# Kernel tuning notes

Measured on AMD Instinct MI355X. Metric: run time of the kernel, lower is better.

Reference implementation:

```python
import jax, jax.numpy as jnp
import numpy as np

N, E, C = 100000, 500000, 128
LN_EPS = 1e-5


def setup_inputs() -> dict:
    key = jax.random.key(0)
    ks = jax.random.split(key, 6)
    x = jax.random.normal(ks[0], (N, C), dtype=jnp.float32)
    edge_index = jax.random.randint(ks[1], (2, E), 0, N, dtype=jnp.int32)
    edge_weight = jax.random.uniform(ks[2], (E,), dtype=jnp.float32)
    scale = 1.0 / np.sqrt(C)
    W1 = jax.random.normal(ks[3], (C, C), dtype=jnp.float32) * scale
    W2 = jax.random.normal(ks[4], (C, C), dtype=jnp.float32) * scale
    b1 = jnp.zeros((C,), jnp.float32)
    b2 = jnp.zeros((C,), jnp.float32)
    g1 = jnp.ones((C,), jnp.float32)
    g2 = jnp.ones((C,), jnp.float32)
    beta1 = jnp.zeros((C,), jnp.float32)
    beta2 = jnp.zeros((C,), jnp.float32)
    return {"x": x, "edge_index": edge_index, "edge_weight": edge_weight,
            "W1": W1, "b1": b1, "g1": g1, "beta1": beta1,
            "W2": W2, "b2": b2, "g2": g2, "beta2": beta2}


def _gcn_norm(edge_index, edge_weight, n):
    # add self loops (weight 1.0), then symmetric deg^{-1/2} normalization;
    # degree() in the source counts edges into col (unweighted), incl. self loops
    src = jnp.concatenate([edge_index[0], jnp.arange(n, dtype=edge_index.dtype)])
    dst = jnp.concatenate([edge_index[1], jnp.arange(n, dtype=edge_index.dtype)])
    ew = jnp.concatenate([edge_weight, jnp.ones((n,), edge_weight.dtype)])
    deg = jax.ops.segment_sum(jnp.ones_like(ew), dst, num_segments=n)
    dis = jnp.where(deg > 0, jax.lax.rsqrt(jnp.maximum(deg, 1.0)) * (deg > 0), 0.0)
    w = dis[src] * ew * dis[dst]
    return src, dst, w


def _layernorm(y, g, b):
    mu = jnp.mean(y, axis=-1, keepdims=True)
    var = jnp.mean(jnp.square(y - mu), axis=-1, keepdims=True)
    return (y - mu) * jax.lax.rsqrt(var + LN_EPS) * g + b


def _gcn_layer(x, W, bias, src, dst, w, n):
    h = x @ W                               # [N,C] linear (no bias)
    msg = w[:, None] * h[src]               # gather + edge scaling [E+N,C]
    out = jax.ops.segment_sum(msg, dst, num_segments=n)  # scatter-add
    return out + bias


def reference(x, edge_index, edge_weight, W1, b1, g1, beta1, W2, b2, g2, beta2):
    n = x.shape[0]
    src, dst, w = _gcn_norm(edge_index, edge_weight, n)
    identity = x
    h = _gcn_layer(x, W1, b1, src, dst, w, n)
    h = jax.nn.gelu(_layernorm(h, g1, beta1), approximate=False)
    h = _gcn_layer(h, W2, b2, src, dst, w, n)
    h = jax.nn.gelu(_layernorm(h, g2, beta2), approximate=False)
    return h + identity
```

## Files before the change

### kernel.cpp

```cpp
#include <hip/hip_runtime.h>
#include <math.h>

#define C 128
#define CAPF 1024
#define CAPA 512

typedef __attribute__((ext_vector_type(8))) short short8;
typedef __attribute__((ext_vector_type(4))) float f32x4;
typedef __attribute__((ext_vector_type(4))) unsigned short ushort4_t;
typedef __attribute__((ext_vector_type(8))) unsigned short ushort8_t;

__device__ inline unsigned short f2b(float f) {
    union { float f; unsigned int u; } v; v.f = f;
    unsigned int u = v.u;
    return (unsigned short)((u + 0x7FFFu + ((u >> 16) & 1u)) >> 16);
}
__device__ inline float bits2f(unsigned int u) {
    union { unsigned int u; float f; } v; v.u = u; return v.f;
}

__device__ inline void acc8(float* a, uint4 u, float s) {
    a[0] += s * bits2f(u.x << 16); a[1] += s * bits2f(u.x & 0xFFFF0000u);
    a[2] += s * bits2f(u.y << 16); a[3] += s * bits2f(u.y & 0xFFFF0000u);
    a[4] += s * bits2f(u.z << 16); a[5] += s * bits2f(u.z & 0xFFFF0000u);
    a[6] += s * bits2f(u.w << 16); a[7] += s * bits2f(u.w & 0xFFFF0000u);
}

__device__ inline void agg_row_lds(
    int row, int c0, int kbeg, int kend, int eb0, int cap,
    const int2* __restrict__ eds, const int2* __restrict__ edata,
    const unsigned short* __restrict__ Hb, const float* __restrict__ dis,
    const float* __restrict__ bias, const float* __restrict__ g,
    const float* __restrict__ beta, float* t) {
    float a[8] = {0.f, 0.f, 0.f, 0.f, 0.f, 0.f, 0.f, 0.f};

    {
        float d = dis[row];
        uint4 hu = *(const uint4*)(Hb + (size_t)row * C + c0);
        acc8(a, hu, d * d);
    }

    const int kc = kend < cap ? kend : cap;
    int k = kbeg;
    for (; k + 3 < kc; k += 4) {
        int2 e0 = eds[k];
        int2 e1 = eds[k + 1];
        int2 e2 = eds[k + 2];
        int2 e3 = eds[k + 3];
        uint4 u0 = *(const uint4*)(Hb + (size_t)e0.x * C + c0);
        uint4 u1 = *(const uint4*)(Hb + (size_t)e1.x * C + c0);
        uint4 u2 = *(const uint4*)(Hb + (size_t)e2.x * C + c0);
        uint4 u3 = *(const uint4*)(Hb + (size_t)e3.x * C + c0);
        acc8(a, u0, bits2f((unsigned int)e0.y));
        acc8(a, u1, bits2f((unsigned int)e1.y));
        acc8(a, u2, bits2f((unsigned int)e2.y));
        acc8(a, u3, bits2f((unsigned int)e3.y));
    }
    for (; k < kc; ++k) {
        int2 e0 = eds[k];
        uint4 u0 = *(const uint4*)(Hb + (size_t)e0.x * C + c0);
        acc8(a, u0, bits2f((unsigned int)e0.y));
    }
    for (; k < kend; ++k) {
        int2 e0 = edata[eb0 + k];
        uint4 u0 = *(const uint4*)(Hb + (size_t)e0.x * C + c0);
        acc8(a, u0, bits2f((unsigned int)e0.y));
    }

    float4 bv0 = *(const float4*)(bias + c0);
    float4 bv1 = *(const float4*)(bias + c0 + 4);
    a[0] += bv0.x; a[1] += bv0.y; a[2] += bv0.z; a[3] += bv0.w;
    a[4] += bv1.x; a[5] += bv1.y; a[6] += bv1.z; a[7] += bv1.w;

    float s = 0.f, sq = 0.f;
    #pragma unroll
    for (int j = 0; j < 8; ++j) { s += a[j]; sq += a[j] * a[j]; }
    #pragma unroll
    for (int off = 8; off >= 1; off >>= 1) {
        s  += __shfl_xor(s, off, 64);
        sq += __shfl_xor(sq, off, 64);
    }
    float mu = s * (1.0f / C);
    float var = sq * (1.0f / C) - mu * mu;
    float rstd = rsqrtf(var + 1e-5f);

    float4 gv0 = *(const float4*)(g + c0);
    float4 gv1 = *(const float4*)(g + c0 + 4);
    float4 be0 = *(const float4*)(beta + c0);
    float4 be1 = *(const float4*)(beta + c0 + 4);
    float gg[8] = {gv0.x, gv0.y, gv0.z, gv0.w, gv1.x, gv1.y, gv1.z, gv1.w};
    float bb[8] = {be0.x, be0.y, be0.z, be0.w, be1.x, be1.y, be1.z, be1.w};

    #pragma unroll
    for (int j = 0; j < 8; ++j) {
        float v = (a[j] - mu) * rstd * gg[j] + bb[j];
        t[j] = 0.5f * v * (1.0f + erff(v * 0.70710678118654752f));
    }
}


__global__ void k_zero(int* __restrict__ cnt, int n) {
    int i = blockIdx.x * blockDim.x + threadIdx.x;
    if (i < n) cnt[i] = 0;
}

__global__ void k_cnt(const int* __restrict__ dst, int* __restrict__ cnt, int e) {
    int i = blockIdx.x * blockDim.x + threadIdx.x;
    if (i < e) atomicAdd(&cnt[dst[i]], 1);
}

__global__ __launch_bounds__(256) void k_scan_a(const int* __restrict__ cnt,
                                                int* __restrict__ rowbeg,
                                                int* __restrict__ blocksum, int n) {
    const int tid = threadIdx.x;
    const int i = blockIdx.x * 256 + tid;
    const int lane = tid & 63, wv = tid >> 6;
    int v = (i < n) ? cnt[i] : 0;
    int x = v;
    #pragma unroll
    for (int off = 1; off < 64; off <<= 1) {
        int y = __shfl_up(x, off, 64);
        if (lane >= off) x += y;
    }
    __shared__ int wsum[4];
    if (lane == 63) wsum[wv] = x;
    __syncthreads();
    int woff = 0;
    #pragma unroll
    for (int k = 0; k < 4; ++k) if (k < wv) woff += wsum[k];
    int incl = x + woff;
    if (i < n) rowbeg[i] = incl - v;
    if (tid == 255) blocksum[blockIdx.x] = incl;
}

__global__ __launch_bounds__(512) void k_scan_b(int* __restrict__ bs, int nb) {
    const int tid = threadIdx.x;
    __shared__ int s[512];
    int v = (tid < nb) ? bs[tid] : 0;
    s[tid] = v;
    __syncthreads();
    for (int off = 1; off < 512; off <<= 1) {
        int t = 0;
        if (tid >= off) t = s[tid - off];
        __syncthreads();
        s[tid] += t;
        __syncthreads();
    }
    if (tid < nb) bs[tid] = s[tid] - v;
}

__global__ void k_scan_c(const int* __restrict__ cnt, const int* __restrict__ bs,
                         int* __restrict__ rowbeg, int* __restrict__ rowcur,
                         float* __restrict__ dis, int n) {
    int i = blockIdx.x * blockDim.x + threadIdx.x;
    if (i >= n) return;
    int rb = rowbeg[i] + bs[i >> 8];
    rowbeg[i] = rb;
    rowcur[i] = rb;
    dis[i] = rsqrtf((float)cnt[i] + 1.0f);
    if (i == n - 1) rowbeg[n] = rb + cnt[i];
}

__global__ void k_place(const int* __restrict__ src, const int* __restrict__ dst,
                        const float* __restrict__ ew, const float* __restrict__ dis,
                        int* __restrict__ rowcur, int2* __restrict__ edata, int e) {
    int i = blockIdx.x * blockDim.x + threadIdx.x;
    if (i >= e) return;
    int s = src[i], d = dst[i];
    int p = atomicAdd(&rowcur[d], 1);
    float w = dis[s] * ew[i] * dis[d];
    union { float f; int i; } wb; wb.f = w;
    edata[p] = make_int2(s, wb.i);
}

__global__ void k_pack_w2(const float* __restrict__ W1, const float* __restrict__ W2,
                          unsigned short* __restrict__ W1p, unsigned short* __restrict__ W2p) {
    int idx = blockIdx.x * blockDim.x + threadIdx.x;
    const float* W = (idx < C * C) ? W1 : W2;
    unsigned short* Wp = (idx < C * C) ? W1p : W2p;
    int p = idx & (C * C - 1);
    int j = p & 7;
    int l = (p >> 3) & 63;
    int t = p >> 9;
    int ks = t & 3, ct = t >> 2;
    int k = ks * 32 + ((l >> 4) << 3) + j;
    int c = (ct << 4) + (l & 15);
    Wp[p] = f2b(W[k * C + c]);
}

__global__ __launch_bounds__(256) void k_gemm_mfma(
    const float* __restrict__ X, const unsigned short* __restrict__ Wp,
    unsigned short* __restrict__ Hb, int n) {
    __shared__ unsigned short xs[32 * C];
    const int tid = threadIdx.x;
    const int base = blockIdx.x * 32;

    const float4* Xv = (const float4*)(X + (size_t)base * C);
    #pragma unroll
    for (int i = 0; i < 4; ++i) {
        int idx4 = i * 256 + tid;
        int elem = idx4 * 4;
        int r = elem >> 7, c = elem & 127;
        float4 v = make_float4(0.f, 0.f, 0.f, 0.f);
        if (base + r < n) v = Xv[idx4];
        ushort4_t pkt;
        pkt.x = f2b(v.x); pkt.y = f2b(v.y); pkt.z = f2b(v.z); pkt.w = f2b(v.w);
        int byte = (r * 256 + c * 2) ^ ((r & 7) << 4);
        *(ushort4_t*)((char*)xs + byte) = pkt;
    }
    __syncthreads();

    const int lane = tid & 63;
    const int wid = tid >> 6;
    const int wm = wid >> 1;
    const int wn = wid & 1;
    const int arow = wm * 16 + (lane & 15);
    const int kg = lane >> 4;

    f32x4 acc[4] = {f32x4{0,0,0,0}, f32x4{0,0,0,0}, f32x4{0,0,0,0}, f32x4{0,0,0,0}};

    #pragma unroll
    for (int ks = 0; ks < 4; ++ks) {
        int abyte = (arow * 256 + ks * 64 + kg * 16) ^ ((arow & 7) << 4);
        short8 a = *(const short8*)((const char*)xs + abyte);
        #pragma unroll
        for (int nt = 0; nt < 4; ++nt) {
            int ct = wn * 4 + nt;
            short8 b = *(const short8*)(Wp + (size_t)((ct * 4 + ks) * 64 + lane) * 8);
            acc[nt] = __builtin_amdgcn_mfma_f32_16x16x32_bf16(a, b, acc[nt], 0, 0, 0);
        }
    }

    const int rbase = base + wm * 16 + kg * 4;
    #pragma unroll
    for (int nt = 0; nt < 4; ++nt) {
        int col = wn * 64 + nt * 16 + (lane & 15);
        #pragma unroll
        for (int r = 0; r < 4; ++r) {
            int row = rbase + r;
            if (row >= n) continue;
            Hb[(size_t)row * C + col] = f2b(acc[nt][r]);
        }
    }
}

__global__ __launch_bounds__(512) void k_fused_agg_gemm(
    const int* __restrict__ rowbeg, const int2* __restrict__ edata,
    const unsigned short* __restrict__ Hb_in, const float* __restrict__ dis,
    const float* __restrict__ bias, const float* __restrict__ g,
    const float* __restrict__ beta,
    const unsigned short* __restrict__ Wp, unsigned short* __restrict__ Hb_out, int n) {
    __shared__ unsigned short xs[32 * C];
    __shared__ int2 eds[CAPF];
    const int tid = threadIdx.x;
    const int lane = tid & 63;
    const int wid = tid >> 6;
    const int grp = lane >> 4;
    const int sub = lane & 15;
    const int base = blockIdx.x * 32;
    const int c0 = sub * 8;

    const int eb0 = rowbeg[base];
    const int top = (base + 32 < n) ? base + 32 : n;
    const int len = rowbeg[top] - eb0;
    const int lcap = len < CAPF ? len : CAPF;
    for (int i = tid; i < lcap; i += 512) eds[i] = edata[eb0 + i];
    __syncthreads();

    {
        int r = wid * 4 + grp;
        int row = base + r;
        float t[8] = {0.f, 0.f, 0.f, 0.f, 0.f, 0.f, 0.f, 0.f};
        if (row < n) {
            int kbeg = rowbeg[row] - eb0;
            int kend = rowbeg[row + 1] - eb0;
            agg_row_lds(row, c0, kbeg, kend, eb0, CAPF, eds, edata,
                        Hb_in, dis, bias, g, beta, t);
        }
        ushort8_t pkt;
        #pragma unroll
        for (int j = 0; j < 8; ++j) pkt[j] = f2b(t[j]);
        int byte = (r * 256 + c0 * 2) ^ ((r & 7) << 4);
        *(ushort8_t*)((char*)xs + byte) = pkt;
    }
    __syncthreads();

    const int wm = wid >> 2;
    const int wn = wid & 3;
    const int arow = wm * 16 + (lane & 15);
    const int kg = lane >> 4;

    f32x4 acc[2] = {f32x4{0,0,0,0}, f32x4{0,0,0,0}};

    #pragma unroll
    for (int ks = 0; ks < 4; ++ks) {
        int abyte = (arow * 256 + ks * 64 + kg * 16) ^ ((arow & 7) << 4);
        short8 a = *(const short8*)((const char*)xs + abyte);
        #pragma unroll
        for (int nt = 0; nt < 2; ++nt) {
            int ct = wn * 2 + nt;
            short8 b = *(const short8*)(Wp + (size_t)((ct * 4 + ks) * 64 + lane) * 8);
            acc[nt] = __builtin_amdgcn_mfma_f32_16x16x32_bf16(a, b, acc[nt], 0, 0, 0);
        }
    }

    const int rbase = base + wm * 16 + kg * 4;
    #pragma unroll
    for (int nt = 0; nt < 2; ++nt) {
        int col = wn * 32 + nt * 16 + (lane & 15);
        #pragma unroll
        for (int r = 0; r < 4; ++r) {
            int row = rbase + r;
            if (row >= n) continue;
            Hb_out[(size_t)row * C + col] = f2b(acc[nt][r]);
        }
    }
}

__global__ __launch_bounds__(256) void k_agg_ln_gelu(
    const int* __restrict__ rowbeg, const int2* __restrict__ edata,
    const unsigned short* __restrict__ Hb, const float* __restrict__ dis,
    const float* __restrict__ bias, const float* __restrict__ g,
    const float* __restrict__ beta, const float* __restrict__ resid,
    float* __restrict__ Out, int n) {
    __shared__ int2 eds[CAPA];
    const int tid = threadIdx.x;
    const int lane = tid & 63;
    const int wid = tid >> 6;
    const int grp = lane >> 4;
    const int sub = lane & 15;
    const int base = blockIdx.x * 16;
    const int c0 = sub * 8;

    const int eb0 = rowbeg[base];
    const int top = (base + 16 < n) ? base + 16 : n;
    const int len = rowbeg[top] - eb0;
    const int lcap = len < CAPA ? len : CAPA;
    for (int i = tid; i < lcap; i += 256) eds[i] = edata[eb0 + i];
    __syncthreads();

    const int row = base + wid * 4 + grp;
    if (row >= n) return;

    int kbeg = rowbeg[row] - eb0;
    int kend = rowbeg[row + 1] - eb0;
    float t[8];
    agg_row_lds(row, c0, kbeg, kend, eb0, CAPA, eds, edata,
                Hb, dis, bias, g, beta, t);

    float4 r0 = *(const float4*)(resid + (size_t)row * C + c0);
    float4 r1 = *(const float4*)(resid + (size_t)row * C + c0 + 4);
    *(float4*)(Out + (size_t)row * C + c0) =
        make_float4(t[0] + r0.x, t[1] + r0.y, t[2] + r0.z, t[3] + r0.w);
    *(float4*)(Out + (size_t)row * C + c0 + 4) =
        make_float4(t[4] + r1.x, t[5] + r1.y, t[6] + r1.z, t[7] + r1.w);
}


extern "C" void kernel_launch(void* const* d_in, const int* in_sizes, int n_in,
                              void* d_out, int out_size, void* d_ws, size_t ws_size,
                              hipStream_t stream) {
    const float* x      = (const float*)d_in[0];
    const int*   eidx   = (const int*)d_in[1];
    const float* ew     = (const float*)d_in[2];
    const float* W1     = (const float*)d_in[3];
    const float* b1     = (const float*)d_in[4];
    const float* g1     = (const float*)d_in[5];
    const float* beta1  = (const float*)d_in[6];
    const float* W2     = (const float*)d_in[7];
    const float* b2     = (const float*)d_in[8];
    const float* g2     = (const float*)d_in[9];
    const float* beta2  = (const float*)d_in[10];

    const int n = in_sizes[0] / C;
    const int e = in_sizes[2];
    const int* src = eidx;
    const int* dst = eidx + e;

    float* out = (float*)d_out;

    char* p = (char*)d_ws;
    auto alloc = [&](size_t bytes) {
        char* q = p;
        p += (bytes + 255) & ~(size_t)255;
        return q;
    };
    float* dis      = (float*)alloc(sizeof(float) * n);
    int*   cnt      = (int*)alloc(sizeof(int) * n);
    int*   rowbeg   = (int*)alloc(sizeof(int) * (n + 1));
    int*   rowcur   = (int*)alloc(sizeof(int) * n);
    int*   blocksum = (int*)alloc(sizeof(int) * 512);
    int2*  edata    = (int2*)alloc(sizeof(int2) * e);
    unsigned short* Hb1 = (unsigned short*)alloc(sizeof(unsigned short) * (size_t)n * C);
    unsigned short* Hb2 = (unsigned short*)alloc(sizeof(unsigned short) * (size_t)n * C);
    unsigned short* W1p = (unsigned short*)alloc(sizeof(unsigned short) * C * C);
    unsigned short* W2p = (unsigned short*)alloc(sizeof(unsigned short) * C * C);

    const int B = 256;
    const int gn = (n + B - 1) / B;
    const int ge = (e + B - 1) / B;

    k_zero<<<gn, B, 0, stream>>>(cnt, n);
    k_cnt<<<ge, B, 0, stream>>>(dst, cnt, e);
    k_scan_a<<<gn, B, 0, stream>>>(cnt, rowbeg, blocksum, n);
    k_scan_b<<<1, 512, 0, stream>>>(blocksum, gn);
    k_scan_c<<<gn, B, 0, stream>>>(cnt, blocksum, rowbeg, rowcur, dis, n);
    k_place<<<ge, B, 0, stream>>>(src, dst, ew, dis, rowcur, edata, e);

    k_pack_w2<<<(2 * C * C) / B, B, 0, stream>>>(W1, W2, W1p, W2p);

    k_gemm_mfma<<<(n + 31) / 32, B, 0, stream>>>(x, W1p, Hb1, n);

    k_fused_agg_gemm<<<(n + 31) / 32, 512, 0, stream>>>(rowbeg, edata, Hb1, dis,
                                                        b1, g1, beta1, W2p, Hb2, n);

    k_agg_ln_gelu<<<(n + 15) / 16, B, 0, stream>>>(rowbeg, edata, Hb2, dis,
                                                   b2, g2, beta2, x, out, n);
}
```

Baseline: 160.3 us.

## Aggregate before GEMM per layer and merge small setup kernels

Each GCN layer now aggregates the bf16 input features first and then applies the weight GEMM, bias, LayerNorm and GELU in one kernel, using the identity A(XW) = (AX)W. The standalone first GEMM and the separate final aggregate kernel are removed. x is converted to bf16 inside the degree-count kernel, and weight packing is folded into the block-sum scan launch, so there are fewer launches and intermediate buffers. The final residual now reads bf16 x instead of fp32, which lowers accuracy slightly. The GEMM output is staged through an extra shared-memory buffer, raising LDS use per block.

```diff
diff --git a/kernel.cpp b/kernel.cpp
--- a/kernel.cpp
+++ b/kernel.cpp
@@ -3,7 +3,7 @@
 
 #define C 128
 #define CAPF 1024
-#define CAPA 512
+#define DSTRIDE 132
 
 typedef __attribute__((ext_vector_type(8))) short short8;
 typedef __attribute__((ext_vector_type(4))) float f32x4;
@@ -26,21 +26,16 @@
     a[6] += s * bits2f(u.w << 16); a[7] += s * bits2f(u.w & 0xFFFF0000u);
 }
 
-__device__ inline void agg_row_lds(
-    int row, int c0, int kbeg, int kend, int eb0, int cap,
+__device__ inline void agg_row_only(
+    int row, int c0, int kbeg, int kend, int eb0,
     const int2* __restrict__ eds, const int2* __restrict__ edata,
-    const unsigned short* __restrict__ Hb, const float* __restrict__ dis,
-    const float* __restrict__ bias, const float* __restrict__ g,
-    const float* __restrict__ beta, float* t) {
-    float a[8] = {0.f, 0.f, 0.f, 0.f, 0.f, 0.f, 0.f, 0.f};
-
+    const unsigned short* __restrict__ Hb, const float* __restrict__ dis, float* a) {
     {
         float d = dis[row];
         uint4 hu = *(const uint4*)(Hb + (size_t)row * C + c0);
         acc8(a, hu, d * d);
     }
-
-    const int kc = kend < cap ? kend : cap;
+    const int kc = kend < CAPF ? kend : CAPF;
     int k = kbeg;
     for (; k + 3 < kc; k += 4) {
         int2 e0 = eds[k];
@@ -66,36 +61,6 @@
         uint4 u0 = *(const uint4*)(Hb + (size_t)e0.x * C + c0);
         acc8(a, u0, bits2f((unsigned int)e0.y));
     }
-
-    float4 bv0 = *(const float4*)(bias + c0);
-    float4 bv1 = *(const float4*)(bias + c0 + 4);
-    a[0] += bv0.x; a[1] += bv0.y; a[2] += bv0.z; a[3] += bv0.w;
-    a[4] += bv1.x; a[5] += bv1.y; a[6] += bv1.z; a[7] += bv1.w;
-
-    float s = 0.f, sq = 0.f;
-    #pragma unroll
-    for (int j = 0; j < 8; ++j) { s += a[j]; sq += a[j] * a[j]; }
-    #pragma unroll
-    for (int off = 8; off >= 1; off >>= 1) {
-        s  += __shfl_xor(s, off, 64);
-        sq += __shfl_xor(sq, off, 64);
-    }
-    float mu = s * (1.0f / C);
-    float var = sq * (1.0f / C) - mu * mu;
-    float rstd = rsqrtf(var + 1e-5f);
-
-    float4 gv0 = *(const float4*)(g + c0);
-    float4 gv1 = *(const float4*)(g + c0 + 4);
-    float4 be0 = *(const float4*)(beta + c0);
-    float4 be1 = *(const float4*)(beta + c0 + 4);
-    float gg[8] = {gv0.x, gv0.y, gv0.z, gv0.w, gv1.x, gv1.y, gv1.z, gv1.w};
-    float bb[8] = {be0.x, be0.y, be0.z, be0.w, be1.x, be1.y, be1.z, be1.w};
-
-    #pragma unroll
-    for (int j = 0; j < 8; ++j) {
-        float v = (a[j] - mu) * rstd * gg[j] + bb[j];
-        t[j] = 0.5f * v * (1.0f + erff(v * 0.70710678118654752f));
-    }
 }
 
 
@@ -104,9 +69,26 @@
     if (i < n) cnt[i] = 0;
 }
 
-__global__ void k_cnt(const int* __restrict__ dst, int* __restrict__ cnt, int e) {
-    int i = blockIdx.x * blockDim.x + threadIdx.x;
-    if (i < e) atomicAdd(&cnt[dst[i]], 1);
+__global__ void k_cnt_cvt(const int* __restrict__ dst, int* __restrict__ cnt, int e, int bc,
+                          const float* __restrict__ x, unsigned short* __restrict__ xb,
+                          int ncvt8) {
+    const int bid = blockIdx.x;
+    const int tid = threadIdx.x;
+    if (bid < bc) {
+        int i = bid * 256 + tid;
+        if (i < ncvt8) {
+            const float4* xp = (const float4*)(x + (size_t)i * 8);
+            float4 v0 = xp[0];
+            float4 v1 = xp[1];
+            ushort8_t pkt;
+            pkt[0] = f2b(v0.x); pkt[1] = f2b(v0.y); pkt[2] = f2b(v0.z); pkt[3] = f2b(v0.w);
+            pkt[4] = f2b(v1.x); pkt[5] = f2b(v1.y); pkt[6] = f2b(v1.z); pkt[7] = f2b(v1.w);
+            *(ushort8_t*)(xb + (size_t)i * 8) = pkt;
+        }
+    } else {
+        int i = (bid - bc) * 256 + tid;
+        if (i < e) atomicAdd(&cnt[dst[i]], 1);
+    }
 }
 
 __global__ __launch_bounds__(256) void k_scan_a(const int* __restrict__ cnt,
@@ -133,20 +115,36 @@
     if (tid == 255) blocksum[blockIdx.x] = incl;
 }
 
-__global__ __launch_bounds__(512) void k_scan_b(int* __restrict__ bs, int nb) {
+__global__ __launch_bounds__(512) void k_scan_b_pack(int* __restrict__ bs, int nb,
+    const float* __restrict__ W1, const float* __restrict__ W2,
+    unsigned short* __restrict__ W1p, unsigned short* __restrict__ W2p) {
     const int tid = threadIdx.x;
-    __shared__ int s[512];
-    int v = (tid < nb) ? bs[tid] : 0;
-    s[tid] = v;
-    __syncthreads();
-    for (int off = 1; off < 512; off <<= 1) {
-        int t = 0;
-        if (tid >= off) t = s[tid - off];
+    if (blockIdx.x == 0) {
+        __shared__ int s[512];
+        int v = (tid < nb) ? bs[tid] : 0;
+        s[tid] = v;
         __syncthreads();
-        s[tid] += t;
-        __syncthreads();
-    }
-    if (tid < nb) bs[tid] = s[tid] - v;
+        for (int off = 1; off < 512; off <<= 1) {
+            int t = 0;
+            if (tid >= off) t = s[tid - off];
+            __syncthreads();
+            s[tid] += t;
+            __syncthreads();
+        }
+        if (tid < nb) bs[tid] = s[tid] - v;
+    } else {
+        int idx = (blockIdx.x - 1) * 512 + tid;
+        const float* W = (idx < C * C) ? W1 : W2;
+        unsigned short* Wp = (idx < C * C) ? W1p : W2p;
+        int p = idx & (C * C - 1);
+        int j = p & 7;
+        int l = (p >> 3) & 63;
+        int t = p >> 9;
+        int ks = t & 3, ct = t >> 2;
+        int k = ks * 32 + ((l >> 4) << 3) + j;
+        int c = (ct << 4) + (l & 15);
+        Wp[p] = f2b(W[k * C + c]);
+    }
 }
 
 __global__ void k_scan_c(const int* __restrict__ cnt, const int* __restrict__ bs,
@@ -173,85 +171,17 @@
     edata[p] = make_int2(s, wb.i);
 }
 
-__global__ void k_pack_w2(const float* __restrict__ W1, const float* __restrict__ W2,
-                          unsigned short* __restrict__ W1p, unsigned short* __restrict__ W2p) {
-    int idx = blockIdx.x * blockDim.x + threadIdx.x;
-    const float* W = (idx < C * C) ? W1 : W2;
-    unsigned short* Wp = (idx < C * C) ? W1p : W2p;
-    int p = idx & (C * C - 1);
-    int j = p & 7;
-    int l = (p >> 3) & 63;
-    int t = p >> 9;
-    int ks = t & 3, ct = t >> 2;
-    int k = ks * 32 + ((l >> 4) << 3) + j;
-    int c = (ct << 4) + (l & 15);
-    Wp[p] = f2b(W[k * C + c]);
-}
-
-__global__ __launch_bounds__(256) void k_gemm_mfma(
-    const float* __restrict__ X, const unsigned short* __restrict__ Wp,
-    unsigned short* __restrict__ Hb, int n) {
-    __shared__ unsigned short xs[32 * C];
-    const int tid = threadIdx.x;
-    const int base = blockIdx.x * 32;
-
-    const float4* Xv = (const float4*)(X + (size_t)base * C);
-    #pragma unroll
-    for (int i = 0; i < 4; ++i) {
-        int idx4 = i * 256 + tid;
-        int elem = idx4 * 4;
-        int r = elem >> 7, c = elem & 127;
-        float4 v = make_float4(0.f, 0.f, 0.f, 0.f);
-        if (base + r < n) v = Xv[idx4];
-        ushort4_t pkt;
-        pkt.x = f2b(v.x); pkt.y = f2b(v.y); pkt.z = f2b(v.z); pkt.w = f2b(v.w);
-        int byte = (r * 256 + c * 2) ^ ((r & 7) << 4);
-        *(ushort4_t*)((char*)xs + byte) = pkt;
-    }
-    __syncthreads();
-
-    const int lane = tid & 63;
-    const int wid = tid >> 6;
-    const int wm = wid >> 1;
-    const int wn = wid & 1;
-    const int arow = wm * 16 + (lane & 15);
-    const int kg = lane >> 4;
-
-    f32x4 acc[4] = {f32x4{0,0,0,0}, f32x4{0,0,0,0}, f32x4{0,0,0,0}, f32x4{0,0,0,0}};
-
-    #pragma unroll
-    for (int ks = 0; ks < 4; ++ks) {
-        int abyte = (arow * 256 + ks * 64 + kg * 16) ^ ((arow & 7) << 4);
-        short8 a = *(const short8*)((const char*)xs + abyte);
-        #pragma unroll
-        for (int nt = 0; nt < 4; ++nt) {
-            int ct = wn * 4 + nt;
-            short8 b = *(const short8*)(Wp + (size_t)((ct * 4 + ks) * 64 + lane) * 8);
-            acc[nt] = __builtin_amdgcn_mfma_f32_16x16x32_bf16(a, b, acc[nt], 0, 0, 0);
-        }
-    }
-
-    const int rbase = base + wm * 16 + kg * 4;
-    #pragma unroll
-    for (int nt = 0; nt < 4; ++nt) {
-        int col = wn * 64 + nt * 16 + (lane & 15);
-        #pragma unroll
-        for (int r = 0; r < 4; ++r) {
-            int row = rbase + r;
-            if (row >= n) continue;
-            Hb[(size_t)row * C + col] = f2b(acc[nt][r]);
-        }
-    }
-}
-
-__global__ __launch_bounds__(512) void k_fused_agg_gemm(
+__global__ __launch_bounds__(512) void k_layer(
     const int* __restrict__ rowbeg, const int2* __restrict__ edata,
-    const unsigned short* __restrict__ Hb_in, const float* __restrict__ dis,
+    const unsigned short* __restrict__ Xin, const float* __restrict__ dis,
+    const unsigned short* __restrict__ Wp,
     const float* __restrict__ bias, const float* __restrict__ g,
     const float* __restrict__ beta,
-    const unsigned short* __restrict__ Wp, unsigned short* __restrict__ Hb_out, int n) {
+    const unsigned short* __restrict__ xb_resid,
+    unsigned short* __restrict__ out_bf16, float* __restrict__ out_f32, int n) {
+    __shared__ int2 eds[CAPF];
     __shared__ unsigned short xs[32 * C];
-    __shared__ int2 eds[CAPF];
+    __shared__ float dacc[32 * DSTRIDE];
     const int tid = threadIdx.x;
     const int lane = tid & 63;
     const int wid = tid >> 6;
@@ -270,90 +200,102 @@
     {
         int r = wid * 4 + grp;
         int row = base + r;
-        float t[8] = {0.f, 0.f, 0.f, 0.f, 0.f, 0.f, 0.f, 0.f};
+        float a[8] = {0.f, 0.f, 0.f, 0.f, 0.f, 0.f, 0.f, 0.f};
         if (row < n) {
             int kbeg = rowbeg[row] - eb0;
             int kend = rowbeg[row + 1] - eb0;
-            agg_row_lds(row, c0, kbeg, kend, eb0, CAPF, eds, edata,
-                        Hb_in, dis, bias, g, beta, t);
+            agg_row_only(row, c0, kbeg, kend, eb0, eds, edata, Xin, dis, a);
         }
         ushort8_t pkt;
         #pragma unroll
-        for (int j = 0; j < 8; ++j) pkt[j] = f2b(t[j]);
+        for (int j = 0; j < 8; ++j) pkt[j] = f2b(a[j]);
         int byte = (r * 256 + c0 * 2) ^ ((r & 7) << 4);
         *(ushort8_t*)((char*)xs + byte) = pkt;
     }
     __syncthreads();
 
-    const int wm = wid >> 2;
-    const int wn = wid & 3;
-    const int arow = wm * 16 + (lane & 15);
-    const int kg = lane >> 4;
-
-    f32x4 acc[2] = {f32x4{0,0,0,0}, f32x4{0,0,0,0}};
-
-    #pragma unroll
-    for (int ks = 0; ks < 4; ++ks) {
-        int abyte = (arow * 256 + ks * 64 + kg * 16) ^ ((arow & 7) << 4);
-        short8 a = *(const short8*)((const char*)xs + abyte);
+    {
+        const int wm = wid >> 2;
+        const int wn = wid & 3;
+        const int arow = wm * 16 + (lane & 15);
+        const int kg = lane >> 4;
+
+        f32x4 acc[2] = {f32x4{0,0,0,0}, f32x4{0,0,0,0}};
+
+        #pragma unroll
+        for (int ks = 0; ks < 4; ++ks) {
+            int abyte = (arow * 256 + ks * 64 + kg * 16) ^ ((arow & 7) << 4);
+            short8 av = *(const short8*)((const char*)xs + abyte);
+            #pragma unroll
+            for (int nt = 0; nt < 2; ++nt) {
+                int ct = wn * 2 + nt;
+                short8 bv = *(const short8*)(Wp + (size_t)((ct * 4 + ks) * 64 + lane) * 8);
+                acc[nt] = __builtin_amdgcn_mfma_f32_16x16x32_bf16(av, bv, acc[nt], 0, 0, 0);
+            }
+        }
+
+        const int rb = wm * 16 + kg * 4;
         #pragma unroll
         for (int nt = 0; nt < 2; ++nt) {
-            int ct = wn * 2 + nt;
-            short8 b = *(const short8*)(Wp + (size_t)((ct * 4 + ks) * 64 + lane) * 8);
-            acc[nt] = __builtin_amdgcn_mfma_f32_16x16x32_bf16(a, b, acc[nt], 0, 0, 0);
-        }
-    }
-
-    const int rbase = base + wm * 16 + kg * 4;
-    #pragma unroll
-    for (int nt = 0; nt < 2; ++nt) {
-        int col = wn * 32 + nt * 16 + (lane & 15);
-        #pragma unroll
-        for (int r = 0; r < 4; ++r) {
-            int row = rbase + r;
-            if (row >= n) continue;
-            Hb_out[(size_t)row * C + col] = f2b(acc[nt][r]);
-        }
-    }
-}
-
-__global__ __launch_bounds__(256) void k_agg_ln_gelu(
-    const int* __restrict__ rowbeg, const int2* __restrict__ edata,
-    const unsigned short* __restrict__ Hb, const float* __restrict__ dis,
-    const float* __restrict__ bias, const float* __restrict__ g,
-    const float* __restrict__ beta, const float* __restrict__ resid,
-    float* __restrict__ Out, int n) {
-    __shared__ int2 eds[CAPA];
-    const int tid = threadIdx.x;
-    const int lane = tid & 63;
-    const int wid = tid >> 6;
-    const int grp = lane >> 4;
-    const int sub = lane & 15;
-    const int base = blockIdx.x * 16;
-    const int c0 = sub * 8;
-
-    const int eb0 = rowbeg[base];
-    const int top = (base + 16 < n) ? base + 16 : n;
-    const int len = rowbeg[top] - eb0;
-    const int lcap = len < CAPA ? len : CAPA;
-    for (int i = tid; i < lcap; i += 256) eds[i] = edata[eb0 + i];
+            int col = wn * 32 + nt * 16 + (lane & 15);
+            float bv = bias[col];
+            #pragma unroll
+            for (int r2 = 0; r2 < 4; ++r2)
+                dacc[(rb + r2) * DSTRIDE + col] = acc[nt][r2] + bv;
+        }
+    }
     __syncthreads();
 
-    const int row = base + wid * 4 + grp;
-    if (row >= n) return;
-
-    int kbeg = rowbeg[row] - eb0;
-    int kend = rowbeg[row + 1] - eb0;
-    float t[8];
-    agg_row_lds(row, c0, kbeg, kend, eb0, CAPA, eds, edata,
-                Hb, dis, bias, g, beta, t);
-
-    float4 r0 = *(const float4*)(resid + (size_t)row * C + c0);
-    float4 r1 = *(const float4*)(resid + (size_t)row * C + c0 + 4);
-    *(float4*)(Out + (size_t)row * C + c0) =
-        make_float4(t[0] + r0.x, t[1] + r0.y, t[2] + r0.z, t[3] + r0.w);
-    *(float4*)(Out + (size_t)row * C + c0 + 4) =
-        make_float4(t[4] + r1.x, t[5] + r1.y, t[6] + r1.z, t[7] + r1.w);
+    {
+        int r = wid * 4 + grp;
+        int row = base + r;
+        if (row >= n) return;
+
+        const float* dp = dacc + r * DSTRIDE + c0;
+        float4 v0 = *(const float4*)(dp);
+        float4 v1 = *(const float4*)(dp + 4);
+        float a[8] = {v0.x, v0.y, v0.z, v0.w, v1.x, v1.y, v1.z, v1.w};
+
+        float s = 0.f, sq = 0.f;
+        #pragma unroll
+        for (int j = 0; j < 8; ++j) { s += a[j]; sq += a[j] * a[j]; }
+        #pragma unroll
+        for (int off = 8; off >= 1; off >>= 1) {
+            s  += __shfl_xor(s, off, 64);
+            sq += __shfl_xor(sq, off, 64);
+        }
+        float mu = s * (1.0f / C);
+        float var = sq * (1.0f / C) - mu * mu;
+        float rstd = rsqrtf(var + 1e-5f);
+
+        float4 gv0 = *(const float4*)(g + c0);
+        float4 gv1 = *(const float4*)(g + c0 + 4);
+        float4 be0 = *(const float4*)(beta + c0);
+        float4 be1 = *(const float4*)(beta + c0 + 4);
+        float gg[8] = {gv0.x, gv0.y, gv0.z, gv0.w, gv1.x, gv1.y, gv1.z, gv1.w};
+        float bb[8] = {be0.x, be0.y, be0.z, be0.w, be1.x, be1.y, be1.z, be1.w};
+
+        float t[8];
+        #pragma unroll
+        for (int j = 0; j < 8; ++j) {
+            float v = (a[j] - mu) * rstd * gg[j] + bb[j];
+            t[j] = 0.5f * v * (1.0f + erff(v * 0.70710678118654752f));
+        }
+
+        if (out_f32 != nullptr) {
+            ushort8_t rv = *(const ushort8_t*)(xb_resid + (size_t)row * C + c0);
+            #pragma unroll
+            for (int j = 0; j < 8; ++j)
+                t[j] += bits2f(((unsigned int)(unsigned short)rv[j]) << 16);
+            *(float4*)(out_f32 + (size_t)row * C + c0) = make_float4(t[0], t[1], t[2], t[3]);
+            *(float4*)(out_f32 + (size_t)row * C + c0 + 4) = make_float4(t[4], t[5], t[6], t[7]);
+        } else {
+            ushort8_t pkt;
+            #pragma unroll
+            for (int j = 0; j < 8; ++j) pkt[j] = f2b(t[j]);
+            *(ushort8_t*)(out_bf16 + (size_t)row * C + c0) = pkt;
+        }
+    }
 }
 
 
@@ -391,29 +333,29 @@
     int*   rowcur   = (int*)alloc(sizeof(int) * n);
     int*   blocksum = (int*)alloc(sizeof(int) * 512);
     int2*  edata    = (int2*)alloc(sizeof(int2) * e);
-    unsigned short* Hb1 = (unsigned short*)alloc(sizeof(unsigned short) * (size_t)n * C);
-    unsigned short* Hb2 = (unsigned short*)alloc(sizeof(unsigned short) * (size_t)n * C);
-    unsigned short* W1p = (unsigned short*)alloc(sizeof(unsigned short) * C * C);
-    unsigned short* W2p = (unsigned short*)alloc(sizeof(unsigned short) * C * C);
+    unsigned short* xb    = (unsigned short*)alloc(sizeof(unsigned short) * (size_t)n * C);
+    unsigned short* hact1 = (unsigned short*)alloc(sizeof(unsigned short) * (size_t)n * C);
+    unsigned short* W1p   = (unsigned short*)alloc(sizeof(unsigned short) * C * C);
+    unsigned short* W2p   = (unsigned short*)alloc(sizeof(unsigned short) * C * C);
 
     const int B = 256;
     const int gn = (n + B - 1) / B;
     const int ge = (e + B - 1) / B;
+    const int ncvt8 = n * C / 8;
+    const int bc = (ncvt8 + B - 1) / B;
 
     k_zero<<<gn, B, 0, stream>>>(cnt, n);
-    k_cnt<<<ge, B, 0, stream>>>(dst, cnt, e);
+    k_cnt_cvt<<<bc + ge, B, 0, stream>>>(dst, cnt, e, bc, x, xb, ncvt8);
     k_scan_a<<<gn, B, 0, stream>>>(cnt, rowbeg, blocksum, n);
-    k_scan_b<<<1, 512, 0, stream>>>(blocksum, gn);
+    k_scan_b_pack<<<1 + (2 * C * C) / 512, 512, 0, stream>>>(blocksum, gn, W1, W2, W1p, W2p);
     k_scan_c<<<gn, B, 0, stream>>>(cnt, blocksum, rowbeg, rowcur, dis, n);
     k_place<<<ge, B, 0, stream>>>(src, dst, ew, dis, rowcur, edata, e);
 
-    k_pack_w2<<<(2 * C * C) / B, B, 0, stream>>>(W1, W2, W1p, W2p);
-
-    k_gemm_mfma<<<(n + 31) / 32, B, 0, stream>>>(x, W1p, Hb1, n);
-
-    k_fused_agg_gemm<<<(n + 31) / 32, 512, 0, stream>>>(rowbeg, edata, Hb1, dis,
-                                                        b1, g1, beta1, W2p, Hb2, n);
-
-    k_agg_ln_gelu<<<(n + 15) / 16, B, 0, stream>>>(rowbeg, edata, Hb2, dis,
-                                                   b2, g2, beta2, x, out, n);
-}
+    k_layer<<<(n + 31) / 32, 512, 0, stream>>>(rowbeg, edata, xb, dis, W1p,
+                                               b1, g1, beta1, nullptr,
+                                               hact1, nullptr, n);
+
+    k_layer<<<(n + 31) / 32, 512, 0, stream>>>(rowbeg, edata, hact1, dis, W2p,
+                                               b2, g2, beta2, xb,
+                                               nullptr, out, n);
+}
```

New measurement: 155.0 us. -3.3%, faster.
